# Kernel tuning notes

Measured on AMD Instinct MI355X. Metric: run time of the kernel, lower is better.

The kernel has to match this reference:

```python
import jax, jax.numpy as jnp
import numpy as np

N = 50000
E = 500000
HID = 64
HEADS = 4
LAYERS = 4
CDIM = 8


def _p(key, shape, scale=0.05):
    return jax.random.normal(key, shape, dtype=jnp.float32) * scale


def setup_inputs() -> dict:
    key = jax.random.key(0)
    ks = jax.random.split(key, 32)
    x = jax.random.normal(ks[0], (N, 8), dtype=jnp.float32)
    src = jax.random.randint(ks[1], (E,), 0, N)
    dst = jax.random.randint(ks[2], (E,), 0, N)
    edge_index = jnp.stack([src, dst]).astype(jnp.int64)
    HC = HEADS * HID
    inp = {
        "x": x,
        "edge_index": edge_index,
        # encoder: Linear(8,64), ELU, Linear(64,64), ELU
        "enc_w1": _p(ks[3], (HID, 8)), "enc_b1": _p(ks[4], (HID,)),
        "enc_w2": _p(ks[5], (HID, HID)), "enc_b2": _p(ks[6], (HID,)),
        # per-layer TransformerConv params, stacked over layers
        "Wq": _p(ks[7], (LAYERS, HC, HID)), "bq": _p(ks[8], (LAYERS, HC)),
        "Wk": _p(ks[9], (LAYERS, HC, HID)), "bk": _p(ks[10], (LAYERS, HC)),
        "Wv": _p(ks[11], (LAYERS, HC, HID)), "bv": _p(ks[12], (LAYERS, HC)),
        "Ws": _p(ks[13], (LAYERS, HID, HID)), "bs": _p(ks[14], (LAYERS, HID)),
        # output MLP: 64->64->32->8
        "out_w1": _p(ks[15], (64, HID)), "out_b1": _p(ks[16], (64,)),
        "out_w2": _p(ks[17], (32, 64)), "out_b2": _p(ks[18], (32,)),
        "out_w3": _p(ks[19], (CDIM, 32)), "out_b3": _p(ks[20], (CDIM,)),
    }
    return inp


def transformer_conv(h, src, dst, Wq, bq, Wk, bk, Wv, bv, Ws, bs):
    """PyG TransformerConv, concat=False, root_weight=True, eval mode (no dropout)."""
    n = h.shape[0]
    q = (h @ Wq.T + bq).reshape(n, HEADS, HID)
    k = (h @ Wk.T + bk).reshape(n, HEADS, HID)
    v = (h @ Wv.T + bv).reshape(n, HEADS, HID)
    # per-edge multi-head scores: (E, H)
    alpha = jnp.einsum("ehd,ehd->eh", q[dst], k[src]) / np.sqrt(HID).astype(np.float32)
    # segment softmax over edges grouped by destination node
    amax = jax.ops.segment_max(alpha, dst, num_segments=n)          # (N, H)
    ex = jnp.exp(alpha - amax[dst])                                 # (E, H)
    denom = jax.ops.segment_sum(ex, dst, num_segments=n)           # (N, H)
    w = ex / denom[dst]                                             # (E, H)
    msg = v[src] * w[:, :, None]                                    # (E, H, C)
    agg = jax.ops.segment_sum(msg, dst, num_segments=n)            # (N, H, C)
    out = agg.mean(axis=1)                                          # concat=False -> head mean
    return out + h @ Ws.T + bs                                      # skip connection


def reference(x, edge_index, enc_w1, enc_b1, enc_w2, enc_b2,
              Wq, bq, Wk, bk, Wv, bv, Ws, bs,
              out_w1, out_b1, out_w2, out_b2, out_w3, out_b3):
    src, dst = edge_index[0], edge_index[1]
    elu = jax.nn.elu
    h = elu(x @ enc_w1.T + enc_b1)
    h = elu(h @ enc_w2.T + enc_b2)
    for l in range(LAYERS):
        h = elu(transformer_conv(h, src, dst, Wq[l], bq[l], Wk[l], bk[l],
                                 Wv[l], bv[l], Ws[l], bs[l]))
        # dropout is identity in eval mode
    o = elu(h @ out_w1.T + out_b1)
    o = elu(o @ out_w2.T + out_b2)
    o = o @ out_w3.T + out_b3
    return o
```

## Files before the change

### kernel.cpp

```cpp
#include <hip/hip_runtime.h>
#include <hip/hip_bf16.h>

#define N_NODES 50000
#define N_EDGES 500000
constexpr int HID = 64;
constexpr int HC  = 256;

typedef unsigned short u16;
typedef unsigned char u8;
typedef __attribute__((ext_vector_type(8))) __bf16 bf16x8;
typedef __attribute__((ext_vector_type(4))) float f32x4;
typedef __attribute__((ext_vector_type(2))) float f32x2;

__device__ __forceinline__ float b2f(u16 u) {
    union { unsigned int i; float f; } c; c.i = ((unsigned int)u) << 16; return c.f;
}
__device__ __forceinline__ u16 f2b(float f) {
    union { float f; unsigned int i; } c; c.f = f;
    unsigned int x = c.i;
    unsigned int lsb = (x >> 16) & 1u;
    x += 0x7fffu + lsb;
    return (u16)(x >> 16);
}
__device__ __forceinline__ float elu_f(float x) { return x > 0.f ? x : expm1f(x); }


__global__ __launch_bounds__(256) void detect_kernel(const int* __restrict__ ei, int* __restrict__ flag) {
    __shared__ int s[4];
    int t = threadIdx.x;
    int nz = ei[2 * t + 1] != 0;
    unsigned long long m = __ballot(nz);
    if ((t & 63) == 0) s[t >> 6] = (m != 0ull) ? 1 : 0;
    __syncthreads();
    if (t == 0) flag[0] = s[0] | s[1] | s[2] | s[3];
}

__global__ __launch_bounds__(256) void wcvt_kernel(const float* __restrict__ Wq, const float* __restrict__ Wk,
                                                   const float* __restrict__ Wv, const float* __restrict__ Wsk,
                                                   u16* __restrict__ w16) {
    int i = blockIdx.x * 256 + threadIdx.x;
    if (i >= 53248) return;
    const float* src; int off;
    if (i < 16384)      { src = Wq;  off = i; }
    else if (i < 32768) { src = Wk;  off = i - 16384; }
    else if (i < 49152) { src = Wv;  off = i - 32768; }
    else                { src = Wsk; off = i - 49152; }
    float4 v = ((const float4*)src)[off];
    ushort4 u; u.x = f2b(v.x); u.y = f2b(v.y); u.z = f2b(v.z); u.w = f2b(v.w);
    ((ushort4*)w16)[i] = u;
}

__global__ __launch_bounds__(256) void hist_kernel(const int* __restrict__ ei, const int* __restrict__ flag,
                                                   int* __restrict__ cnt) {
    int e = blockIdx.x * 256 + threadIdx.x;
    if (e < N_EDGES) {
        int d = flag[0] ? ei[N_EDGES + e] : ei[2 * N_EDGES + 2 * e];
        atomicAdd(&cnt[d], 1);
    }
}

__global__ __launch_bounds__(512) void scan1_kernel(const int* __restrict__ cnt,
                                                    int* __restrict__ row_start, int* __restrict__ bsum) {
    __shared__ int sc[512];
    int t = threadIdx.x;
    int i = blockIdx.x * 512 + t;
    int v = (i < N_NODES) ? cnt[i] : 0;
    sc[t] = v;
    __syncthreads();
    for (int off = 1; off < 512; off <<= 1) {
        int u = (t >= off) ? sc[t - off] : 0;
        __syncthreads();
        sc[t] += u;
        __syncthreads();
    }
    if (i < N_NODES) row_start[i] = sc[t] - v;
    if (t == 511) bsum[blockIdx.x] = sc[511];
}

__global__ __launch_bounds__(128) void scan2_kernel(int* __restrict__ bsum, int* __restrict__ row_start) {
    __shared__ int sc[128];
    const int NB = (N_NODES + 511) / 512;
    int t = threadIdx.x;
    int v = (t < NB) ? bsum[t] : 0;
    sc[t] = v;
    __syncthreads();
    for (int off = 1; off < 128; off <<= 1) {
        int u = (t >= off) ? sc[t - off] : 0;
        __syncthreads();
        sc[t] += u;
        __syncthreads();
    }
    if (t < NB) bsum[t] = sc[t] - v;
    if (t == 127) row_start[N_NODES] = sc[127];
}

__global__ __launch_bounds__(512) void scan3_kernel(int* __restrict__ row_start, const int* __restrict__ bsum) {
    int i = blockIdx.x * 512 + threadIdx.x;
    if (i < N_NODES) row_start[i] += bsum[blockIdx.x];
}

__global__ __launch_bounds__(256) void scatter_kernel(const int* __restrict__ ei, const int* __restrict__ flag,
                                const int* __restrict__ row_start, int* __restrict__ cursor,
                                int* __restrict__ csr_src) {
    int e = blockIdx.x * 256 + threadIdx.x;
    if (e < N_EDGES) {
        int isI32 = flag[0];
        int s = isI32 ? ei[e] : ei[2 * e];
        int d = isI32 ? ei[N_EDGES + e] : ei[2 * N_EDGES + 2 * e];
        int pos = row_start[d] + atomicAdd(&cursor[d], 1);
        csr_src[pos] = s;
    }
}

__global__ __launch_bounds__(256) void encoder_kernel(const float* __restrict__ x,
                               const float* __restrict__ w1, const float* __restrict__ b1,
                               const float* __restrict__ w2, const float* __restrict__ b2,
                               u16* __restrict__ h) {
    __shared__ float xs[64 * 9];
    __shared__ float w1s[64 * 9];
    __shared__ u16 t1s[64 * 72];
    __shared__ u16 w2s[64 * 72];
    __shared__ float b1s[64], b2s[64];
    int t = threadIdx.x;
    int m0 = blockIdx.x * 64;

    if (t < 128) {
        int row = t >> 1, c = (t & 1) * 4;
        float4 val = make_float4(0.f, 0.f, 0.f, 0.f);
        if (m0 + row < N_NODES) val = *(const float4*)(x + (size_t)(m0 + row) * 8 + c);
        *(float4*)&xs[row * 9 + c] = val;
    }
    if (t >= 128 && t < 256) {
        int p = t - 128;
        int row = p >> 1, c = (p & 1) * 4;
        float4 val = *(const float4*)(w1 + row * 8 + c);
        *(float4*)&w1s[row * 9 + c] = val;
    }
    #pragma unroll
    for (int r = 0; r < 4; ++r) {
        int p = t + r * 256; int row = p >> 4, kc = (p & 15) * 4;
        float4 val = *(const float4*)(w2 + row * 64 + kc);
        ushort4 u; u.x = f2b(val.x); u.y = f2b(val.y); u.z = f2b(val.z); u.w = f2b(val.w);
        *(ushort4*)&w2s[row * 72 + kc] = u;
    }
    if (t < 64) { b1s[t] = b1[t]; b2s[t] = b2[t]; }
    __syncthreads();

    {
        int j = t & 63, sub = t >> 6;
        #pragma unroll
        for (int g = 0; g < 16; ++g) {
            int node = g * 4 + sub;
            float acc = b1s[j];
            #pragma unroll
            for (int m = 0; m < 8; ++m) acc += xs[node * 9 + m] * w1s[j * 9 + m];
            t1s[node * 72 + j] = f2b(elu_f(acc));
        }
    }
    __syncthreads();

    int wave = t >> 6, lane = t & 63;
    int lrow = lane & 15, quad = lane >> 4;
    int m_off = wave * 16;
    bf16x8 a0 = *(const bf16x8*)&t1s[(m_off + lrow) * 72 + quad * 8];
    bf16x8 a1 = *(const bf16x8*)&t1s[(m_off + lrow) * 72 + 32 + quad * 8];
    #pragma unroll
    for (int nsub = 0; nsub < 4; ++nsub) {
        bf16x8 b0 = *(const bf16x8*)&w2s[(nsub * 16 + lrow) * 72 + quad * 8];
        bf16x8 b1v = *(const bf16x8*)&w2s[(nsub * 16 + lrow) * 72 + 32 + quad * 8];
        f32x4 acc = {0.f, 0.f, 0.f, 0.f};
        acc = __builtin_amdgcn_mfma_f32_16x16x32_bf16(a0, b0, acc, 0, 0, 0);
        acc = __builtin_amdgcn_mfma_f32_16x16x32_bf16(a1, b1v, acc, 0, 0, 0);
        int col = nsub * 16 + lrow;
        float bias = b2s[col];
        #pragma unroll
        for (int r = 0; r < 4; ++r) {
            int row = m0 + m_off + quad * 4 + r;
            if (row < N_NODES) h[(size_t)row * 64 + col] = f2b(elu_f(acc[r] + bias));
        }
    }
}

__global__ __launch_bounds__(256) void proj_kernel(const u16* __restrict__ h,
    const u16* __restrict__ wq16, const u16* __restrict__ wk16,
    const u16* __restrict__ wv16, const u16* __restrict__ wsk16,
    const float* __restrict__ bq, const float* __restrict__ bk,
    const float* __restrict__ bv, const float* __restrict__ bsk,
    int layer,
    u16* __restrict__ q, u8* __restrict__ kv, float* __restrict__ skip)
{
    __shared__ u16 wsA[64 * 72];
    __shared__ u16 wsB[64 * 72];
    __shared__ float pool[64 * 68];
    u16* qst  = (u16*)pool;
    u8*  kvst = (u8*)pool;
    float* skst = pool;

    int t = threadIdx.x;
    int m0 = blockIdx.x * 64;
    int wave = t >> 6, lane = t & 63;
    int lrow = lane & 15, quad = lane >> 4;
    int nl = wave * 16 + lrow;

    const u16* Wq16  = wq16  + (size_t)layer * HC * HID;
    const u16* Wk16  = wk16  + (size_t)layer * HC * HID;
    const u16* Wv16  = wv16  + (size_t)layer * HC * HID;
    const u16* Wsk16 = wsk16 + (size_t)layer * HID * HID;
    const float* bqL  = bq  + layer * HC;
    const float* bkL  = bk  + layer * HC;
    const float* bvL  = bv  + layer * HC;
    const float* bskL = bsk + layer * HID;

    #pragma unroll
    for (int it = 0; it < 2; ++it) {
        int p = t + it * 256; int row = p >> 3, kc = (p & 7) * 8;
        uint4 val = make_uint4(0u, 0u, 0u, 0u);
        if (m0 + row < N_NODES) val = *(const uint4*)(h + (size_t)(m0 + row) * 64 + kc);
        *(uint4*)&wsA[row * 72 + kc] = val;
    }
    __syncthreads();
    bf16x8 a0 = *(const bf16x8*)&wsA[(wave * 16 + lrow) * 72 + quad * 8];
    bf16x8 a1 = *(const bf16x8*)&wsA[(wave * 16 + lrow) * 72 + 32 + quad * 8];

    auto stageIssue = [&](const u16* W, int cb, uint4& r0, uint4& r1) {
        const u16* sp = W + (size_t)(cb + (t >> 3)) * 64 + (t & 7) * 8;
        r0 = *(const uint4*)sp;
        r1 = *(const uint4*)(sp + 2048);
    };
    auto stageWrite = [&](u16* buf, uint4 r0, uint4 r1) {
        int row = t >> 3, kc = (t & 7) * 8;
        *(uint4*)&buf[row * 72 + kc] = r0;
        *(uint4*)&buf[(row + 32) * 72 + kc] = r1;
    };

    auto computeQ = [&](int ct, const u16* BUF) {
        #pragma unroll
        for (int nsub = 0; nsub < 4; ++nsub) {
            bf16x8 w0 = *(const bf16x8*)&BUF[(nsub * 16 + lrow) * 72 + quad * 8];
            bf16x8 w1 = *(const bf16x8*)&BUF[(nsub * 16 + lrow) * 72 + 32 + quad * 8];
            f32x4 acc = {0.f, 0.f, 0.f, 0.f};
            acc = __builtin_amdgcn_mfma_f32_16x16x32_bf16(w0, a0, acc, 0, 0, 0);
            acc = __builtin_amdgcn_mfma_f32_16x16x32_bf16(w1, a1, acc, 0, 0, 0);
            float4 b4 = *(const float4*)(bqL + ct * 64 + nsub * 16 + quad * 4);
            ushort4 o;
            o.x = f2b(acc[0] + b4.x); o.y = f2b(acc[1] + b4.y);
            o.z = f2b(acc[2] + b4.z); o.w = f2b(acc[3] + b4.w);
            *(ushort4*)&qst[nl * 72 + nsub * 16 + quad * 4] = o;
        }
    };
    auto computeKV = [&](int ct, const u16* BUF, const float* bias, int voff) {
        #pragma unroll
        for (int nsub = 0; nsub < 4; ++nsub) {
            bf16x8 w0 = *(const bf16x8*)&BUF[(nsub * 16 + lrow) * 72 + quad * 8];
            bf16x8 w1 = *(const bf16x8*)&BUF[(nsub * 16 + lrow) * 72 + 32 + quad * 8];
            f32x4 acc = {0.f, 0.f, 0.f, 0.f};
            acc = __builtin_amdgcn_mfma_f32_16x16x32_bf16(w0, a0, acc, 0, 0, 0);
            acc = __builtin_amdgcn_mfma_f32_16x16x32_bf16(w1, a1, acc, 0, 0, 0);
            float4 b4 = *(const float4*)(bias + ct * 64 + nsub * 16 + quad * 4);
            float f0 = (acc[0] + b4.x) * 16.f, f1 = (acc[1] + b4.y) * 16.f;
            float f2v = (acc[2] + b4.z) * 16.f, f3v = (acc[3] + b4.w) * 16.f;
            int pk = __builtin_amdgcn_cvt_pk_fp8_f32(f0, f1, 0, false);
            pk = __builtin_amdgcn_cvt_pk_fp8_f32(f2v, f3v, pk, true);
            int g = nsub * 4 + quad;
            *(unsigned int*)&kvst[nl * 144 + g * 8 + voff] = (unsigned int)pk;
        }
    };
    auto computeSK = [&](const u16* BUF) {
        #pragma unroll
        for (int nsub = 0; nsub < 4; ++nsub) {
            bf16x8 w0 = *(const bf16x8*)&BUF[(nsub * 16 + lrow) * 72 + quad * 8];
            bf16x8 w1 = *(const bf16x8*)&BUF[(nsub * 16 + lrow) * 72 + 32 + quad * 8];
            f32x4 acc = {0.f, 0.f, 0.f, 0.f};
            acc = __builtin_amdgcn_mfma_f32_16x16x32_bf16(w0, a0, acc, 0, 0, 0);
            acc = __builtin_amdgcn_mfma_f32_16x16x32_bf16(w1, a1, acc, 0, 0, 0);
            float4 b4 = *(const float4*)(bskL + nsub * 16 + quad * 4);
            float4 o;
            o.x = acc[0] + b4.x; o.y = acc[1] + b4.y;
            o.z = acc[2] + b4.z; o.w = acc[3] + b4.w;
            *(float4*)&skst[nl * 68 + nsub * 16 + quad * 4] = o;
        }
    };
    auto flushQ = [&](int ct) {
        #pragma unroll
        for (int it = 0; it < 2; ++it) {
            int p = t + it * 256; int row = p >> 3, ch = p & 7;
            int grow = m0 + row;
            if (grow < N_NODES)
                *(uint4*)(q + (size_t)grow * 256 + ct * 64 + ch * 8) = *(const uint4*)&qst[row * 72 + ch * 8];
        }
    };
    auto flushKV = [&](int ct) {
        #pragma unroll
        for (int it = 0; it < 2; ++it) {
            int p = t + it * 256; int row = p >> 3, ch = p & 7;
            int grow = m0 + row;
            if (grow < N_NODES)
                *(uint4*)(kv + (size_t)grow * 512 + ct * 128 + ch * 16) = *(const uint4*)&kvst[row * 144 + ch * 16];
        }
    };

    {
        uint4 r0, r1;
        stageIssue(Wq16, 0, r0, r1);
        stageWrite(wsB, r0, r1);
    }
    __syncthreads();

    uint4 r0, r1;
    stageIssue(Wq16, 64, r0, r1);  computeQ(0, wsB);          __syncthreads(); flushQ(0);  stageWrite(wsA, r0, r1); __syncthreads();
    stageIssue(Wq16, 128, r0, r1); computeQ(1, wsA);          __syncthreads(); flushQ(1);  stageWrite(wsB, r0, r1); __syncthreads();
    stageIssue(Wq16, 192, r0, r1); computeQ(2, wsB);          __syncthreads(); flushQ(2);  stageWrite(wsA, r0, r1); __syncthreads();
    stageIssue(Wk16, 0, r0, r1);   computeQ(3, wsA);          __syncthreads(); flushQ(3);  stageWrite(wsB, r0, r1); __syncthreads();
    stageIssue(Wv16, 0, r0, r1);   computeKV(0, wsB, bkL, 0); __syncthreads();             stageWrite(wsA, r0, r1); __syncthreads();
    stageIssue(Wk16, 64, r0, r1);  computeKV(0, wsA, bvL, 4); __syncthreads(); flushKV(0); stageWrite(wsB, r0, r1); __syncthreads();
    stageIssue(Wv16, 64, r0, r1);  computeKV(1, wsB, bkL, 0); __syncthreads();             stageWrite(wsA, r0, r1); __syncthreads();
    stageIssue(Wk16, 128, r0, r1); computeKV(1, wsA, bvL, 4); __syncthreads(); flushKV(1); stageWrite(wsB, r0, r1); __syncthreads();
    stageIssue(Wv16, 128, r0, r1); computeKV(2, wsB, bkL, 0); __syncthreads();             stageWrite(wsA, r0, r1); __syncthreads();
    stageIssue(Wk16, 192, r0, r1); computeKV(2, wsA, bvL, 4); __syncthreads(); flushKV(2); stageWrite(wsB, r0, r1); __syncthreads();
    stageIssue(Wv16, 192, r0, r1); computeKV(3, wsB, bkL, 0); __syncthreads();             stageWrite(wsA, r0, r1); __syncthreads();
    stageIssue(Wsk16, 0, r0, r1);  computeKV(3, wsA, bvL, 4); __syncthreads(); flushKV(3); stageWrite(wsB, r0, r1); __syncthreads();

    computeSK(wsB);
    __syncthreads();
    {
        int row = t >> 2, c0 = (t & 3) * 16;
        int grow = m0 + row;
        if (grow < N_NODES) {
            #pragma unroll
            for (int j = 0; j < 4; ++j)
                *(float4*)(skip + (size_t)grow * 64 + c0 + j * 4) = *(const float4*)&skst[row * 68 + c0 + j * 4];
        }
    }
}

#define ATTN_QUAD(S0q, S1q, S2q, S3q, V1, V2, V3) do { \
    uint2 c0 = *(const uint2*)(kvl + (size_t)(unsigned)(S0q) * 512); \
    uint2 c1 = *(const uint2*)(kvl + (size_t)(unsigned)(S1q) * 512); \
    uint2 c2 = *(const uint2*)(kvl + (size_t)(unsigned)(S2q) * 512); \
    uint2 c3 = *(const uint2*)(kvl + (size_t)(unsigned)(S3q) * 512); \
    f32x2 k0a = __builtin_amdgcn_cvt_pk_f32_fp8(c0.x, false), k0b = __builtin_amdgcn_cvt_pk_f32_fp8(c0.x, true); \
    f32x2 k1a = __builtin_amdgcn_cvt_pk_f32_fp8(c1.x, false), k1b = __builtin_amdgcn_cvt_pk_f32_fp8(c1.x, true); \
    f32x2 k2a = __builtin_amdgcn_cvt_pk_f32_fp8(c2.x, false), k2b = __builtin_amdgcn_cvt_pk_f32_fp8(c2.x, true); \
    f32x2 k3a = __builtin_amdgcn_cvt_pk_f32_fp8(c3.x, false), k3b = __builtin_amdgcn_cvt_pk_f32_fp8(c3.x, true); \
    f32x2 pd0 = qlo * k0a + qhi * k0b; \
    f32x2 pd1 = qlo * k1a + qhi * k1b; \
    f32x2 pd2 = qlo * k2a + qhi * k2b; \
    f32x2 pd3 = qlo * k3a + qhi * k3b; \
    float p0 = pd0.x + pd0.y, p1 = pd1.x + pd1.y, p2 = pd2.x + pd2.y, p3 = pd3.x + pd3.y; \
    p0 += __shfl_xor(p0, 1); p1 += __shfl_xor(p1, 1); p2 += __shfl_xor(p2, 1); p3 += __shfl_xor(p3, 1); \
    p0 += __shfl_xor(p0, 2); p1 += __shfl_xor(p1, 2); p2 += __shfl_xor(p2, 2); p3 += __shfl_xor(p3, 2); \
    p0 += __shfl_xor(p0, 4); p1 += __shfl_xor(p1, 4); p2 += __shfl_xor(p2, 4); p3 += __shfl_xor(p3, 4); \
    p0 += __shfl_xor(p0, 8); p1 += __shfl_xor(p1, 8); p2 += __shfl_xor(p2, 8); p3 += __shfl_xor(p3, 8); \
    float w0 = __expf(p0 * SC); \
    float w1 = (V1) ? __expf(p1 * SC) : 0.f; \
    float w2 = (V2) ? __expf(p2 * SC) : 0.f; \
    float w3 = (V3) ? __expf(p3 * SC) : 0.f; \
    l += (w0 + w1) + (w2 + w3); \
    f32x2 v0a = __builtin_amdgcn_cvt_pk_f32_fp8(c0.y, false), v0b = __builtin_amdgcn_cvt_pk_f32_fp8(c0.y, true); \
    f32x2 v1a = __builtin_amdgcn_cvt_pk_f32_fp8(c1.y, false), v1b = __builtin_amdgcn_cvt_pk_f32_fp8(c1.y, true); \
    f32x2 v2a = __builtin_amdgcn_cvt_pk_f32_fp8(c2.y, false), v2b = __builtin_amdgcn_cvt_pk_f32_fp8(c2.y, true); \
    f32x2 v3a = __builtin_amdgcn_cvt_pk_f32_fp8(c3.y, false), v3b = __builtin_amdgcn_cvt_pk_f32_fp8(c3.y, true); \
    accA += v0a * w0; accA += v1a * w1; accA += v2a * w2; accA += v3a * w3; \
    accB += v0b * w0; accB += v1b * w1; accB += v2b * w2; accB += v3b * w3; \
} while (0)

__global__ __launch_bounds__(256) void attn_kernel(
    const u16* __restrict__ q, const u8* __restrict__ kv,
    const float* __restrict__ skip,
    const int* __restrict__ row_start, const int* __restrict__ csr_src,
    u16* __restrict__ hout)
{
    __shared__ int s_lds[4][64];
    int wave = threadIdx.x >> 6;
    int lane = threadIdx.x & 63;
    int n = blockIdx.x * 4 + wave;
    if (n >= N_NODES) return;
    ushort4 q4 = ((const ushort4*)(q + (size_t)n * 256))[lane];
    f32x2 qlo = { b2f(q4.x), b2f(q4.y) };
    f32x2 qhi = { b2f(q4.z), b2f(q4.w) };
    const u8* kvl = kv + lane * 8;
    const float SC = 0.0078125f;
    float l = 0.f;
    f32x2 accA = {0.f, 0.f};
    f32x2 accB = {0.f, 0.f};
    int e0 = row_start[n];
    int deg = row_start[n + 1] - e0;

    for (int base = 0; base < deg; base += 64) {
        int rem = deg - base;
        int m = rem < 64 ? rem : 64;
        int li = lane < m ? lane : m - 1;
        s_lds[wave][lane] = csr_src[e0 + base + li];
        int i = 0;
        for (; i + 4 <= m; i += 4) {
            int4 sq = *(const int4*)&s_lds[wave][i];
            ATTN_QUAD(sq.x, sq.y, sq.z, sq.w, 1, 1, 1);
        }
        if (i < m) {
            int4 sq = *(const int4*)&s_lds[wave][i];
            int rem2 = m - i;
            int sB = rem2 > 1 ? sq.y : sq.x;
            int sC = rem2 > 2 ? sq.z : sq.x;
            ATTN_QUAD(sq.x, sB, sC, sq.x, rem2 > 1, rem2 > 2, 0);
        }
    }

    float inv = l > 0.f ? 1.f / l : 0.f;
    float a0 = accA.x * inv, a1 = accA.y * inv;
    float a2 = accB.x * inv, a3 = accB.y * inv;
    a0 += __shfl_xor(a0, 16); a0 += __shfl_xor(a0, 32);
    a1 += __shfl_xor(a1, 16); a1 += __shfl_xor(a1, 32);
    a2 += __shfl_xor(a2, 16); a2 += __shfl_xor(a2, 32);
    a3 += __shfl_xor(a3, 16); a3 += __shfl_xor(a3, 32);
    if ((lane >> 4) == 0) {
        const float OS = 0.015625f;
        float4 sk = ((const float4*)(skip + (size_t)n * 64))[lane];
        ushort4 o;
        o.x = f2b(elu_f(OS * a0 + sk.x));
        o.y = f2b(elu_f(OS * a1 + sk.y));
        o.z = f2b(elu_f(OS * a2 + sk.z));
        o.w = f2b(elu_f(OS * a3 + sk.w));
        ((ushort4*)(hout + (size_t)n * 64))[lane] = o;
    }
}

__global__ __launch_bounds__(256) void mlp_kernel(const u16* __restrict__ h,
    const float* __restrict__ w1, const float* __restrict__ b1,
    const float* __restrict__ w2, const float* __restrict__ b2,
    const float* __restrict__ w3, const float* __restrict__ b3,
    float* __restrict__ out)
{
    __shared__ u16 hs[64 * 72];
    __shared__ u16 w1s[64 * 72];
    __shared__ u16 t1s[64 * 72];
    __shared__ u16 w2s[32 * 72];
    __shared__ float t2s[64 * 33];
    __shared__ float w3s[8 * 33];
    __shared__ float b1s[64], b2s[32], b3s[8];
    int t = threadIdx.x;
    int m0 = blockIdx.x * 64;

    #pragma unroll
    for (int it = 0; it < 2; ++it) {
        int p = t + it * 256; int row = p >> 3, kc = (p & 7) * 8;
        uint4 val = make_uint4(0u, 0u, 0u, 0u);
        if (m0 + row < N_NODES) val = *(const uint4*)(h + (size_t)(m0 + row) * 64 + kc);
        *(uint4*)&hs[row * 72 + kc] = val;
    }
    #pragma unroll
    for (int r = 0; r < 4; ++r) {
        int p = t + r * 256; int row = p >> 4, kc = (p & 15) * 4;
        float4 val = *(const float4*)(w1 + row * 64 + kc);
        ushort4 u; u.x = f2b(val.x); u.y = f2b(val.y); u.z = f2b(val.z); u.w = f2b(val.w);
        *(ushort4*)&w1s[row * 72 + kc] = u;
    }
    #pragma unroll
    for (int r = 0; r < 2; ++r) {
        int p = t + r * 256; int row = p >> 4, kc = (p & 15) * 4;
        float4 val = *(const float4*)(w2 + row * 64 + kc);
        ushort4 u; u.x = f2b(val.x); u.y = f2b(val.y); u.z = f2b(val.z); u.w = f2b(val.w);
        *(ushort4*)&w2s[row * 72 + kc] = u;
    }
    if (t < 8 * 32) { int r = t >> 5, c = t & 31; w3s[r * 33 + c] = w3[t]; }
    if (t < 64) b1s[t] = b1[t];
    if (t >= 64 && t < 96) b2s[t - 64] = b2[t - 64];
    if (t >= 96 && t < 104) b3s[t - 96] = b3[t - 96];
    __syncthreads();

    int wave = t >> 6, lane = t & 63;
    int lrow = lane & 15, quad = lane >> 4;
    int m_off = wave * 16;

    {
        bf16x8 a0 = *(const bf16x8*)&hs[(m_off + lrow) * 72 + quad * 8];
        bf16x8 a1 = *(const bf16x8*)&hs[(m_off + lrow) * 72 + 32 + quad * 8];
        #pragma unroll
        for (int nsub = 0; nsub < 4; ++nsub) {
            bf16x8 b0 = *(const bf16x8*)&w1s[(nsub * 16 + lrow) * 72 + quad * 8];
            bf16x8 b1v = *(const bf16x8*)&w1s[(nsub * 16 + lrow) * 72 + 32 + quad * 8];
            f32x4 acc = {0.f, 0.f, 0.f, 0.f};
            acc = __builtin_amdgcn_mfma_f32_16x16x32_bf16(a0, b0, acc, 0, 0, 0);
            acc = __builtin_amdgcn_mfma_f32_16x16x32_bf16(a1, b1v, acc, 0, 0, 0);
            int col = nsub * 16 + lrow;
            float bias = b1s[col];
            #pragma unroll
            for (int r = 0; r < 4; ++r) {
                int row = m_off + quad * 4 + r;
                t1s[row * 72 + col] = f2b(elu_f(acc[r] + bias));
            }
        }
    }
    __syncthreads();

    {
        bf16x8 a0 = *(const bf16x8*)&t1s[(m_off + lrow) * 72 + quad * 8];
        bf16x8 a1 = *(const bf16x8*)&t1s[(m_off + lrow) * 72 + 32 + quad * 8];
        #pragma unroll
        for (int nsub = 0; nsub < 2; ++nsub) {
            bf16x8 b0 = *(const bf16x8*)&w2s[(nsub * 16 + lrow) * 72 + quad * 8];
            bf16x8 b1v = *(const bf16x8*)&w2s[(nsub * 16 + lrow) * 72 + 32 + quad * 8];
            f32x4 acc = {0.f, 0.f, 0.f, 0.f};
            acc = __builtin_amdgcn_mfma_f32_16x16x32_bf16(a0, b0, acc, 0, 0, 0);
            acc = __builtin_amdgcn_mfma_f32_16x16x32_bf16(a1, b1v, acc, 0, 0, 0);
            int col = nsub * 16 + lrow;
            float bias = b2s[col];
            #pragma unroll
            for (int r = 0; r < 4; ++r) {
                int row = m_off + quad * 4 + r;
                t2s[row * 33 + col] = elu_f(acc[r] + bias);
            }
        }
    }
    __syncthreads();

    #pragma unroll
    for (int r = 0; r < 2; ++r) {
        int idx = t + r * 256;
        int node = idx >> 3, j = idx & 7;
        int row = m0 + node;
        if (row < N_NODES) {
            float acc = b3s[j];
            #pragma unroll
            for (int kk = 0; kk < 32; ++kk) acc += t2s[node * 33 + kk] * w3s[j * 33 + kk];
            out[(size_t)row * 8 + j] = acc;
        }
    }
}

extern "C" void kernel_launch(void* const* d_in, const int* in_sizes, int n_in,
                              void* d_out, int out_size, void* d_ws, size_t ws_size,
                              hipStream_t stream) {
    (void)in_sizes; (void)n_in; (void)out_size; (void)ws_size;
    const float* x   = (const float*)d_in[0];
    const int* ei    = (const int*)d_in[1];
    const float* ew1 = (const float*)d_in[2];
    const float* eb1 = (const float*)d_in[3];
    const float* ew2 = (const float*)d_in[4];
    const float* eb2 = (const float*)d_in[5];
    const float* Wq  = (const float*)d_in[6];
    const float* bq  = (const float*)d_in[7];
    const float* Wk  = (const float*)d_in[8];
    const float* bk  = (const float*)d_in[9];
    const float* Wv  = (const float*)d_in[10];
    const float* bv  = (const float*)d_in[11];
    const float* Wsk = (const float*)d_in[12];
    const float* bsk = (const float*)d_in[13];
    const float* ow1 = (const float*)d_in[14];
    const float* ob1 = (const float*)d_in[15];
    const float* ow2 = (const float*)d_in[16];
    const float* ob2 = (const float*)d_in[17];
    const float* ow3 = (const float*)d_in[18];
    const float* ob3 = (const float*)d_in[19];

    char* ws = (char*)d_ws;
    size_t off = 0;
    auto alloc = [&](size_t bytes) -> void* {
        void* p = ws + off;
        off += (bytes + 255) & ~(size_t)255;
        return p;
    };
    u16*   h0    = (u16*)  alloc((size_t)N_NODES * 64 * 2);
    u16*   h1    = (u16*)  alloc((size_t)N_NODES * 64 * 2);
    u16*   q     = (u16*)  alloc((size_t)N_NODES * 256 * 2);
    u8*    kv    = (u8*)   alloc((size_t)N_NODES * 512);
    float* skp   = (float*)alloc((size_t)N_NODES * 64 * 4);
    u16*   w16   = (u16*)  alloc((size_t)212992 * 2);
    int*   cnt   = (int*)  alloc((size_t)N_NODES * 4);
    int*   cursor= (int*)  alloc((size_t)N_NODES * 4);
    int*   rowst = (int*)  alloc((size_t)(N_NODES + 1) * 4);
    int*   csr   = (int*)  alloc((size_t)N_EDGES * 4);
    int*   bsum  = (int*)  alloc(512);
    int*   flag  = (int*)  alloc(256);

    u16* wq16  = w16;
    u16* wk16  = w16 + 65536;
    u16* wv16  = w16 + 131072;
    u16* wsk16 = w16 + 196608;

    const int NB = (N_NODES + 511) / 512;

    hipMemsetAsync(cnt, 0, 2 * 200192, stream);
    detect_kernel<<<1, 256, 0, stream>>>(ei, flag);
    wcvt_kernel<<<208, 256, 0, stream>>>(Wq, Wk, Wv, Wsk, w16);
    hist_kernel<<<(N_EDGES + 255) / 256, 256, 0, stream>>>(ei, flag, cnt);
    scan1_kernel<<<NB, 512, 0, stream>>>(cnt, rowst, bsum);
    scan2_kernel<<<1, 128, 0, stream>>>(bsum, rowst);
    scan3_kernel<<<NB, 512, 0, stream>>>(rowst, bsum);
    scatter_kernel<<<(N_EDGES + 255) / 256, 256, 0, stream>>>(ei, flag, rowst, cursor, csr);

    encoder_kernel<<<(N_NODES + 63) / 64, 256, 0, stream>>>(x, ew1, eb1, ew2, eb2, h0);

    u16* hin = h0;
    u16* hout = h1;
    for (int l = 0; l < 4; ++l) {
        proj_kernel<<<(N_NODES + 63) / 64, 256, 0, stream>>>(hin, wq16, wk16, wv16, wsk16,
                                                             bq, bk, bv, bsk, l, q, kv, skp);
        attn_kernel<<<(N_NODES + 3) / 4, 256, 0, stream>>>(q, kv, skp, rowst, csr, hout);
        u16* tmp = hin; hin = hout; hout = tmp;
    }

    mlp_kernel<<<(N_NODES + 63) / 64, 256, 0, stream>>>(hin, ow1, ob1, ow2, ob2, ow3, ob3, (float*)d_out);
}
```

Before: 456.1 us.

## Double proj rows per block and use DPP reductions in attention

```diff
diff --git a/kernel.cpp b/kernel.cpp
--- a/kernel.cpp
+++ b/kernel.cpp
@@ -191,16 +191,17 @@
 {
     __shared__ u16 wsA[64 * 72];
     __shared__ u16 wsB[64 * 72];
-    __shared__ float pool[64 * 68];
+    __shared__ float pool[128 * 68];
     u16* qst  = (u16*)pool;
     u8*  kvst = (u8*)pool;
     float* skst = pool;
 
     int t = threadIdx.x;
-    int m0 = blockIdx.x * 64;
+    int m0 = blockIdx.x * 128;
     int wave = t >> 6, lane = t & 63;
     int lrow = lane & 15, quad = lane >> 4;
-    int nl = wave * 16 + lrow;
+    int nl0 = wave * 16 + lrow;
+    int nl1 = 64 + nl0;
 
     const u16* Wq16  = wq16  + (size_t)layer * HC * HID;
     const u16* Wk16  = wk16  + (size_t)layer * HC * HID;
@@ -211,17 +212,6 @@
     const float* bvL  = bv  + layer * HC;
     const float* bskL = bsk + layer * HID;
 
-    #pragma unroll
-    for (int it = 0; it < 2; ++it) {
-        int p = t + it * 256; int row = p >> 3, kc = (p & 7) * 8;
-        uint4 val = make_uint4(0u, 0u, 0u, 0u);
-        if (m0 + row < N_NODES) val = *(const uint4*)(h + (size_t)(m0 + row) * 64 + kc);
-        *(uint4*)&wsA[row * 72 + kc] = val;
-    }
-    __syncthreads();
-    bf16x8 a0 = *(const bf16x8*)&wsA[(wave * 16 + lrow) * 72 + quad * 8];
-    bf16x8 a1 = *(const bf16x8*)&wsA[(wave * 16 + lrow) * 72 + 32 + quad * 8];
-
     auto stageIssue = [&](const u16* W, int cb, uint4& r0, uint4& r1) {
         const u16* sp = W + (size_t)(cb + (t >> 3)) * 64 + (t & 7) * 8;
         r0 = *(const uint4*)sp;
@@ -233,19 +223,50 @@
         *(uint4*)&buf[(row + 32) * 72 + kc] = r1;
     };
 
+    uint4 hv[4];
+    #pragma unroll
+    for (int it = 0; it < 4; ++it) {
+        int p = t + it * 256; int row = p >> 3, kc = (p & 7) * 8;
+        hv[it] = make_uint4(0u, 0u, 0u, 0u);
+        if (m0 + row < N_NODES) hv[it] = *(const uint4*)(h + (size_t)(m0 + row) * 64 + kc);
+    }
+    uint4 q0r0, q0r1;
+    stageIssue(Wq16, 0, q0r0, q0r1);
+    #pragma unroll
+    for (int it = 0; it < 4; ++it) {
+        int p = t + it * 256; int row = p >> 3, kc = (p & 7) * 8;
+        if (row < 64) *(uint4*)&wsA[row * 72 + kc] = hv[it];
+        else          *(uint4*)&wsB[(row - 64) * 72 + kc] = hv[it];
+    }
+    __syncthreads();
+    bf16x8 a0 = *(const bf16x8*)&wsA[nl0 * 72 + quad * 8];
+    bf16x8 a1 = *(const bf16x8*)&wsA[nl0 * 72 + 32 + quad * 8];
+    bf16x8 a2 = *(const bf16x8*)&wsB[nl0 * 72 + quad * 8];
+    bf16x8 a3 = *(const bf16x8*)&wsB[nl0 * 72 + 32 + quad * 8];
+    __syncthreads();
+    stageWrite(wsB, q0r0, q0r1);
+    __syncthreads();
+
     auto computeQ = [&](int ct, const u16* BUF) {
         #pragma unroll
         for (int nsub = 0; nsub < 4; ++nsub) {
             bf16x8 w0 = *(const bf16x8*)&BUF[(nsub * 16 + lrow) * 72 + quad * 8];
             bf16x8 w1 = *(const bf16x8*)&BUF[(nsub * 16 + lrow) * 72 + 32 + quad * 8];
+            float4 b4 = *(const float4*)(bqL + ct * 64 + nsub * 16 + quad * 4);
             f32x4 acc = {0.f, 0.f, 0.f, 0.f};
             acc = __builtin_amdgcn_mfma_f32_16x16x32_bf16(w0, a0, acc, 0, 0, 0);
             acc = __builtin_amdgcn_mfma_f32_16x16x32_bf16(w1, a1, acc, 0, 0, 0);
-            float4 b4 = *(const float4*)(bqL + ct * 64 + nsub * 16 + quad * 4);
             ushort4 o;
             o.x = f2b(acc[0] + b4.x); o.y = f2b(acc[1] + b4.y);
             o.z = f2b(acc[2] + b4.z); o.w = f2b(acc[3] + b4.w);
-            *(ushort4*)&qst[nl * 72 + nsub * 16 + quad * 4] = o;
+            *(ushort4*)&qst[nl0 * 72 + nsub * 16 + quad * 4] = o;
+            f32x4 acc2 = {0.f, 0.f, 0.f, 0.f};
+            acc2 = __builtin_amdgcn_mfma_f32_16x16x32_bf16(w0, a2, acc2, 0, 0, 0);
+            acc2 = __builtin_amdgcn_mfma_f32_16x16x32_bf16(w1, a3, acc2, 0, 0, 0);
+            ushort4 o2;
+            o2.x = f2b(acc2[0] + b4.x); o2.y = f2b(acc2[1] + b4.y);
+            o2.z = f2b(acc2[2] + b4.z); o2.w = f2b(acc2[3] + b4.w);
+            *(ushort4*)&qst[nl1 * 72 + nsub * 16 + quad * 4] = o2;
         }
     };
     auto computeKV = [&](int ct, const u16* BUF, const float* bias, int voff) {
@@ -253,16 +274,28 @@
         for (int nsub = 0; nsub < 4; ++nsub) {
             bf16x8 w0 = *(const bf16x8*)&BUF[(nsub * 16 + lrow) * 72 + quad * 8];
             bf16x8 w1 = *(const bf16x8*)&BUF[(nsub * 16 + lrow) * 72 + 32 + quad * 8];
+            float4 b4 = *(const float4*)(bias + ct * 64 + nsub * 16 + quad * 4);
+            int g = nsub * 4 + quad;
             f32x4 acc = {0.f, 0.f, 0.f, 0.f};
             acc = __builtin_amdgcn_mfma_f32_16x16x32_bf16(w0, a0, acc, 0, 0, 0);
             acc = __builtin_amdgcn_mfma_f32_16x16x32_bf16(w1, a1, acc, 0, 0, 0);
-            float4 b4 = *(const float4*)(bias + ct * 64 + nsub * 16 + quad * 4);
-            float f0 = (acc[0] + b4.x) * 16.f, f1 = (acc[1] + b4.y) * 16.f;
-            float f2v = (acc[2] + b4.z) * 16.f, f3v = (acc[3] + b4.w) * 16.f;
-            int pk = __builtin_amdgcn_cvt_pk_fp8_f32(f0, f1, 0, false);
-            pk = __builtin_amdgcn_cvt_pk_fp8_f32(f2v, f3v, pk, true);
-            int g = nsub * 4 + quad;
-            *(unsigned int*)&kvst[nl * 144 + g * 8 + voff] = (unsigned int)pk;
+            {
+                float f0 = (acc[0] + b4.x) * 16.f, f1 = (acc[1] + b4.y) * 16.f;
+                float f2v = (acc[2] + b4.z) * 16.f, f3v = (acc[3] + b4.w) * 16.f;
+                int pk = __builtin_amdgcn_cvt_pk_fp8_f32(f0, f1, 0, false);
+                pk = __builtin_amdgcn_cvt_pk_fp8_f32(f2v, f3v, pk, true);
+                *(unsigned int*)&kvst[nl0 * 144 + g * 8 + voff] = (unsigned int)pk;
+            }
+            f32x4 acc2 = {0.f, 0.f, 0.f, 0.f};
+            acc2 = __builtin_amdgcn_mfma_f32_16x16x32_bf16(w0, a2, acc2, 0, 0, 0);
+            acc2 = __builtin_amdgcn_mfma_f32_16x16x32_bf16(w1, a3, acc2, 0, 0, 0);
+            {
+                float f0 = (acc2[0] + b4.x) * 16.f, f1 = (acc2[1] + b4.y) * 16.f;
+                float f2v = (acc2[2] + b4.z) * 16.f, f3v = (acc2[3] + b4.w) * 16.f;
+                int pk = __builtin_amdgcn_cvt_pk_fp8_f32(f0, f1, 0, false);
+                pk = __builtin_amdgcn_cvt_pk_fp8_f32(f2v, f3v, pk, true);
+                *(unsigned int*)&kvst[nl1 * 144 + g * 8 + voff] = (unsigned int)pk;
+            }
         }
     };
     auto computeSK = [&](const u16* BUF) {
@@ -270,19 +303,26 @@
         for (int nsub = 0; nsub < 4; ++nsub) {
             bf16x8 w0 = *(const bf16x8*)&BUF[(nsub * 16 + lrow) * 72 + quad * 8];
             bf16x8 w1 = *(const bf16x8*)&BUF[(nsub * 16 + lrow) * 72 + 32 + quad * 8];
+            float4 b4 = *(const float4*)(bskL + nsub * 16 + quad * 4);
             f32x4 acc = {0.f, 0.f, 0.f, 0.f};
             acc = __builtin_amdgcn_mfma_f32_16x16x32_bf16(w0, a0, acc, 0, 0, 0);
             acc = __builtin_amdgcn_mfma_f32_16x16x32_bf16(w1, a1, acc, 0, 0, 0);
-            float4 b4 = *(const float4*)(bskL + nsub * 16 + quad * 4);
             float4 o;
             o.x = acc[0] + b4.x; o.y = acc[1] + b4.y;
             o.z = acc[2] + b4.z; o.w = acc[3] + b4.w;
-            *(float4*)&skst[nl * 68 + nsub * 16 + quad * 4] = o;
+            *(float4*)&skst[nl0 * 68 + nsub * 16 + quad * 4] = o;
+            f32x4 acc2 = {0.f, 0.f, 0.f, 0.f};
+            acc2 = __builtin_amdgcn_mfma_f32_16x16x32_bf16(w0, a2, acc2, 0, 0, 0);
+            acc2 = __builtin_amdgcn_mfma_f32_16x16x32_bf16(w1, a3, acc2, 0, 0, 0);
+            float4 o2;
+            o2.x = acc2[0] + b4.x; o2.y = acc2[1] + b4.y;
+            o2.z = acc2[2] + b4.z; o2.w = acc2[3] + b4.w;
+            *(float4*)&skst[nl1 * 68 + nsub * 16 + quad * 4] = o2;
         }
     };
     auto flushQ = [&](int ct) {
         #pragma unroll
-        for (int it = 0; it < 2; ++it) {
+        for (int it = 0; it < 4; ++it) {
             int p = t + it * 256; int row = p >> 3, ch = p & 7;
             int grow = m0 + row;
             if (grow < N_NODES)
@@ -291,20 +331,13 @@
     };
     auto flushKV = [&](int ct) {
         #pragma unroll
-        for (int it = 0; it < 2; ++it) {
+        for (int it = 0; it < 4; ++it) {
             int p = t + it * 256; int row = p >> 3, ch = p & 7;
             int grow = m0 + row;
             if (grow < N_NODES)
                 *(uint4*)(kv + (size_t)grow * 512 + ct * 128 + ch * 16) = *(const uint4*)&kvst[row * 144 + ch * 16];
         }
     };
-
-    {
-        uint4 r0, r1;
-        stageIssue(Wq16, 0, r0, r1);
-        stageWrite(wsB, r0, r1);
-    }
-    __syncthreads();
 
     uint4 r0, r1;
     stageIssue(Wq16, 64, r0, r1);  computeQ(0, wsB);          __syncthreads(); flushQ(0);  stageWrite(wsA, r0, r1); __syncthreads();
@@ -322,8 +355,9 @@
 
     computeSK(wsB);
     __syncthreads();
-    {
-        int row = t >> 2, c0 = (t & 3) * 16;
+    #pragma unroll
+    for (int it = 0; it < 2; ++it) {
+        int p = t + it * 256; int row = p >> 2, c0 = (p & 3) * 16;
         int grow = m0 + row;
         if (grow < N_NODES) {
             #pragma unroll
@@ -332,6 +366,9 @@
         }
     }
 }
+
+#define DPP_ADD(x, ctrl) ((x) + __builtin_bit_cast(float, \
+    __builtin_amdgcn_update_dpp(0, __builtin_bit_cast(int, (x)), (ctrl), 0xf, 0xf, true)))
 
 #define ATTN_QUAD(S0q, S1q, S2q, S3q, V1, V2, V3) do { \
     uint2 c0 = *(const uint2*)(kvl + (size_t)(unsigned)(S0q) * 512); \
@@ -347,10 +384,10 @@
     f32x2 pd2 = qlo * k2a + qhi * k2b; \
     f32x2 pd3 = qlo * k3a + qhi * k3b; \
     float p0 = pd0.x + pd0.y, p1 = pd1.x + pd1.y, p2 = pd2.x + pd2.y, p3 = pd3.x + pd3.y; \
-    p0 += __shfl_xor(p0, 1); p1 += __shfl_xor(p1, 1); p2 += __shfl_xor(p2, 1); p3 += __shfl_xor(p3, 1); \
-    p0 += __shfl_xor(p0, 2); p1 += __shfl_xor(p1, 2); p2 += __shfl_xor(p2, 2); p3 += __shfl_xor(p3, 2); \
-    p0 += __shfl_xor(p0, 4); p1 += __shfl_xor(p1, 4); p2 += __shfl_xor(p2, 4); p3 += __shfl_xor(p3, 4); \
-    p0 += __shfl_xor(p0, 8); p1 += __shfl_xor(p1, 8); p2 += __shfl_xor(p2, 8); p3 += __shfl_xor(p3, 8); \
+    p0 = DPP_ADD(p0, 0xB1);  p1 = DPP_ADD(p1, 0xB1);  p2 = DPP_ADD(p2, 0xB1);  p3 = DPP_ADD(p3, 0xB1);  \
+    p0 = DPP_ADD(p0, 0x4E);  p1 = DPP_ADD(p1, 0x4E);  p2 = DPP_ADD(p2, 0x4E);  p3 = DPP_ADD(p3, 0x4E);  \
+    p0 = DPP_ADD(p0, 0x141); p1 = DPP_ADD(p1, 0x141); p2 = DPP_ADD(p2, 0x141); p3 = DPP_ADD(p3, 0x141); \
+    p0 = DPP_ADD(p0, 0x140); p1 = DPP_ADD(p1, 0x140); p2 = DPP_ADD(p2, 0x140); p3 = DPP_ADD(p3, 0x140); \
     float w0 = __expf(p0 * SC); \
     float w1 = (V1) ? __expf(p1 * SC) : 0.f; \
     float w2 = (V2) ? __expf(p2 * SC) : 0.f; \
@@ -593,8 +630,8 @@
     u16* hin = h0;
     u16* hout = h1;
     for (int l = 0; l < 4; ++l) {
-        proj_kernel<<<(N_NODES + 63) / 64, 256, 0, stream>>>(hin, wq16, wk16, wv16, wsk16,
-                                                             bq, bk, bv, bsk, l, q, kv, skp);
+        proj_kernel<<<(N_NODES + 127) / 128, 256, 0, stream>>>(hin, wq16, wk16, wv16, wsk16,
+                                                               bq, bk, bv, bsk, l, q, kv, skp);
         attn_kernel<<<(N_NODES + 3) / 4, 256, 0, stream>>>(q, kv, skp, rowst, csr, hout);
         u16* tmp = hin; hin = hout; hout = tmp;
     }
```

Result: faster. 441.7 us (-3.1%).
